# Optimization experiments

Measured on AMD Instinct MI355X. Metric: run time of the kernel, lower is better.

The kernel has to match this reference:

```python
import jax, jax.numpy as jnp
import numpy as np

DIM = 768
HEADS = 12
HEAD_DIM = DIM // HEADS
MAX_LEN = 2048
EPS = 1e-5

def layer_norm(x, w, b):
    mu = jnp.mean(x, axis=-1, keepdims=True)
    var = jnp.var(x, axis=-1, keepdims=True)
    return (x - mu) * jax.lax.rsqrt(var + EPS) * w + b


def setup_inputs() -> dict:
    key = jax.random.key(0)
    ks = jax.random.split(key, 16)
    B, N = 2, 2048
    s = 1.0 / np.sqrt(DIM)
    inp = {
        "visible_features": jax.random.normal(ks[0], (B, N, DIM), jnp.float32),
        "infrared_features": jax.random.normal(ks[1], (B, N, DIM), jnp.float32),
        "wq": jax.random.normal(ks[2], (DIM, DIM), jnp.float32) * s,
        "bq": jnp.zeros((DIM,), jnp.float32),
        "lnq_w": jnp.ones((DIM,), jnp.float32),
        "lnq_b": jnp.zeros((DIM,), jnp.float32),
        "wk": jax.random.normal(ks[3], (DIM, DIM), jnp.float32) * s,
        "bk": jnp.zeros((DIM,), jnp.float32),
        "lnk_w": jnp.ones((DIM,), jnp.float32),
        "lnk_b": jnp.zeros((DIM,), jnp.float32),
        "wv": jax.random.normal(ks[4], (DIM, DIM), jnp.float32) * s,
        "bv": jnp.zeros((DIM,), jnp.float32),
        "lnv_w": jnp.ones((DIM,), jnp.float32),
        "lnv_b": jnp.zeros((DIM,), jnp.float32),
        "pos_emb": jax.random.normal(ks[5], (MAX_LEN, DIM), jnp.float32),
        "wo": jax.random.normal(ks[6], (DIM, DIM), jnp.float32) * s,
        "bo": jnp.zeros((DIM,), jnp.float32),
        "gate_w": jax.random.normal(ks[7], (DIM, 2 * DIM), jnp.float32) * (1.0 / np.sqrt(2 * DIM)),
        "gate_b": jnp.zeros((DIM,), jnp.float32),
        "ln_w": jnp.ones((DIM,), jnp.float32),
        "ln_b": jnp.zeros((DIM,), jnp.float32),
    }
    return inp


def reference(visible_features, infrared_features, wq, bq, lnq_w, lnq_b,
              wk, bk, lnk_w, lnk_b, wv, bv, lnv_w, lnv_b,
              pos_emb, wo, bo, gate_w, gate_b, ln_w, ln_b):
    B, N, _ = visible_features.shape
    scale = HEAD_DIM ** -0.5

    def proj_heads(x, w, b, gw, gb):
        y = layer_norm(x @ w.T + b, gw, gb)  # [B,N,D]
        return y.reshape(B, N, HEADS, HEAD_DIM).transpose(0, 2, 1, 3)  # [B,H,N,d]

    q = proj_heads(infrared_features, wq, bq, lnq_w, lnq_b)
    k = proj_heads(visible_features, wk, bk, lnk_w, lnk_b)
    v = proj_heads(visible_features, wv, bv, lnv_w, lnv_b)

    pos = pos_emb[:N].reshape(1, N, HEADS, HEAD_DIM).transpose(0, 2, 1, 3)  # [1,H,N,d]

    scores = jnp.einsum('bhnd,bhmd->bhnm', q, k) * scale
    scores = scores + jnp.einsum('bhnd,xhmd->bhnm', q, pos)
    attn = jax.nn.softmax(scores, axis=-1)  # dropout is identity in eval

    out = jnp.einsum('bhnm,bhmd->bhnd', attn, v)
    out = out.transpose(0, 2, 1, 3).reshape(B, N, DIM)
    out = out @ wo.T + bo

    gate = jax.nn.sigmoid(jnp.concatenate([visible_features, out], axis=-1) @ gate_w.T + gate_b)
    fused = visible_features * gate + out * (1.0 - gate)
    return layer_norm(fused, ln_w, ln_b)
```

## Files before the change

kernel.cpp:

```cpp
#include <hip/hip_runtime.h>
#include <hip/hip_bf16.h>

#define DIMC 768
#define NSEQ 2048
#define NB 2
#define NH 12
#define HD 64
#define EPSLN 1e-5f

typedef __attribute__((ext_vector_type(8))) short     bf16x8;
typedef __attribute__((ext_vector_type(8))) unsigned short ushort8;
typedef __attribute__((ext_vector_type(4))) unsigned short ushort4v;
typedef __attribute__((ext_vector_type(4))) float     f32x4;

__device__ __forceinline__ unsigned short f2b(float f) {
    union { float f; unsigned u; } x; x.f = f;
    unsigned r = x.u + 0x7fffu + ((x.u >> 16) & 1u);
    return (unsigned short)(r >> 16);
}

#define MFMA16(a, b, c) __builtin_amdgcn_mfma_f32_16x16x32_bf16((a), (b), (c), 0, 0, 0)

__global__ __launch_bounds__(256)
void cast_all_kernel(const float* __restrict__ wq, const float* __restrict__ wk,
                     const float* __restrict__ wv, const float* __restrict__ wo,
                     const float* __restrict__ gw, const float* __restrict__ vis,
                     const float* __restrict__ inf_,
                     unsigned short* __restrict__ o_wq, unsigned short* __restrict__ o_wk,
                     unsigned short* __restrict__ o_wv, unsigned short* __restrict__ o_wo,
                     unsigned short* __restrict__ o_gw, unsigned short* __restrict__ o_vis,
                     unsigned short* __restrict__ o_inf)
{
    const int g = blockIdx.x * 256 + threadIdx.x;
    const int W = 147456;
    const float* src; unsigned short* dst; int off;
    if      (g < 1*W)            { src = wq;   dst = o_wq;  off = g;          }
    else if (g < 2*W)            { src = wk;   dst = o_wk;  off = g - 1*W;    }
    else if (g < 3*W)            { src = wv;   dst = o_wv;  off = g - 2*W;    }
    else if (g < 4*W)            { src = wo;   dst = o_wo;  off = g - 3*W;    }
    else if (g < 4*W + 294912)   { src = gw;   dst = o_gw;  off = g - 4*W;    }
    else if (g < 4*W + 1081344)  { src = vis;  dst = o_vis; off = g - 4*W - 294912; }
    else                         { src = inf_; dst = o_inf; off = g - 4*W - 1081344; }
    f32x4 v = ((const f32x4*)src)[off];
    ushort4v t;
    t[0] = f2b(v[0]); t[1] = f2b(v[1]); t[2] = f2b(v[2]); t[3] = f2b(v[3]);
    ((ushort4v*)dst)[off] = t;
}

template<int ACC, int WBF>
__global__ __launch_bounds__(256)
void gemm_bf16_kernel(const unsigned short* __restrict__ A,
                      const unsigned short* __restrict__ W,
                      const float* __restrict__ bias,
                      float* __restrict__ C,
                      unsigned short* __restrict__ Cb,
                      int ldw)
{
    __shared__ unsigned short As[64][72];
    __shared__ unsigned short Bs[64][72];
    const int m0 = blockIdx.x * 64, n0 = blockIdx.y * 64;
    const int lane = threadIdx.x & 63, wid = threadIdx.x >> 6;
    const int wm = wid >> 1, wn = wid & 1;
    const int r16 = lane & 15, kg = lane >> 4;

    f32x4 acc[2][2] = {};

    const int sr = threadIdx.x >> 2;
    const int sc = (threadIdx.x & 3) * 16;
    const size_t arow = (size_t)(m0 + sr) * DIMC;
    const size_t brow = (size_t)(n0 + sr) * (size_t)ldw;

    for (int k0 = 0; k0 < DIMC; k0 += 64) {
        ushort8 a0 = *(const ushort8*)&A[arow + k0 + sc];
        ushort8 a1 = *(const ushort8*)&A[arow + k0 + sc + 8];
        ushort8 b0 = *(const ushort8*)&W[brow + k0 + sc];
        ushort8 b1 = *(const ushort8*)&W[brow + k0 + sc + 8];
        if (k0) __syncthreads();
        *(ushort8*)&As[sr][sc]     = a0;
        *(ushort8*)&As[sr][sc + 8] = a1;
        *(ushort8*)&Bs[sr][sc]     = b0;
        *(ushort8*)&Bs[sr][sc + 8] = b1;
        __syncthreads();
        #pragma unroll
        for (int ks = 0; ks < 2; ++ks) {
            bf16x8 af0 = *(const bf16x8*)&As[wm*32 +      r16][ks*32 + kg*8];
            bf16x8 af1 = *(const bf16x8*)&As[wm*32 + 16 + r16][ks*32 + kg*8];
            bf16x8 bg0 = *(const bf16x8*)&Bs[wn*32 +      r16][ks*32 + kg*8];
            bf16x8 bg1 = *(const bf16x8*)&Bs[wn*32 + 16 + r16][ks*32 + kg*8];
            acc[0][0] = MFMA16(af0, bg0, acc[0][0]);
            acc[0][1] = MFMA16(af0, bg1, acc[0][1]);
            acc[1][0] = MFMA16(af1, bg0, acc[1][0]);
            acc[1][1] = MFMA16(af1, bg1, acc[1][1]);
        }
    }

    #pragma unroll
    for (int mi = 0; mi < 2; ++mi)
    #pragma unroll
    for (int nj = 0; nj < 2; ++nj) {
        const int gr = m0 + wm*32 + mi*16 + kg*4;
        const int gc = n0 + wn*32 + nj*16 + r16;
        const float bv = bias ? bias[gc] : 0.f;
        #pragma unroll
        for (int r = 0; r < 4; ++r) {
            const size_t idx = (size_t)(gr + r) * DIMC + gc;
            float v = acc[mi][nj][r] + bv;
            if (ACC) v += C[idx];
            C[idx] = v;
            if (WBF) Cb[idx] = f2b(v);
        }
    }
}

template<int MODE>
__global__ __launch_bounds__(256)
void ln_bf16_kernel(const float* __restrict__ Z,
                    const float* __restrict__ w,
                    const float* __restrict__ b,
                    const float* __restrict__ pos,
                    unsigned short* __restrict__ out)
{
    const int row = blockIdx.x;
    const int n = row & (NSEQ - 1);
    float x[3];
    float s = 0.f, q = 0.f;
    #pragma unroll
    for (int u = 0; u < 3; ++u) {
        const int j = threadIdx.x + u * 256;
        x[u] = Z[(size_t)row * DIMC + j];
        s += x[u];
        q += x[u] * x[u];
    }
    #pragma unroll
    for (int off = 32; off > 0; off >>= 1) {
        s += __shfl_down(s, off);
        q += __shfl_down(q, off);
    }
    __shared__ float ls[8];
    const int wv_ = threadIdx.x >> 6;
    if ((threadIdx.x & 63) == 0) { ls[wv_] = s; ls[4 + wv_] = q; }
    __syncthreads();
    if (threadIdx.x == 0) {
        ls[0] = ls[0] + ls[1] + ls[2] + ls[3];
        ls[4] = ls[4] + ls[5] + ls[6] + ls[7];
    }
    __syncthreads();
    const float mu  = ls[0] * (1.f / DIMC);
    const float var = ls[4] * (1.f / DIMC) - mu * mu;
    const float rs  = rsqrtf(var + EPSLN);
    #pragma unroll
    for (int u = 0; u < 3; ++u) {
        const int j = threadIdx.x + u * 256;
        float y = (x[u] - mu) * rs * w[j] + b[j];
        if (MODE == 1) y = y * 0.125f + pos[(size_t)n * DIMC + j];
        out[(size_t)row * DIMC + j] = f2b(y);
    }
}

__global__ __launch_bounds__(256)
void attn_bf16_kernel(const unsigned short* __restrict__ Q,
                      const unsigned short* __restrict__ K,
                      const unsigned short* __restrict__ V,
                      unsigned short* __restrict__ O)
{
    __shared__ unsigned short Ks[64][72];
    __shared__ unsigned short Vt[64][72];
    __shared__ unsigned short Ps[4][16][72];

    const int bh = blockIdx.x;
    const int b = bh / NH, h = bh % NH;
    const int n0 = blockIdx.y * 64;
    const int lane = threadIdx.x & 63, w = threadIdx.x >> 6;
    const int r16 = lane & 15, kg = lane >> 4;

    const size_t base = (size_t)b * NSEQ * DIMC + (size_t)h * HD;

    const size_t qoff = base + (size_t)(n0 + w * 16 + r16) * DIMC + kg * 8;
    bf16x8 aq0 = *(const bf16x8*)&Q[qoff];
    bf16x8 aq1 = *(const bf16x8*)&Q[qoff + 32];

    f32x4 o[4] = {};
    float mrow[4] = {-1e30f, -1e30f, -1e30f, -1e30f};
    float lrow[4] = {};

    for (int m0 = 0; m0 < NSEQ; m0 += 64) {
        __syncthreads();
        {
            const int kv = threadIdx.x >> 2;
            const int c  = (threadIdx.x & 3) * 16;
            const size_t go = base + (size_t)(m0 + kv) * DIMC + c;
            *(ushort8*)&Ks[kv][c]     = *(const ushort8*)&K[go];
            *(ushort8*)&Ks[kv][c + 8] = *(const ushort8*)&K[go + 8];
        }
        {
            const int kv = threadIdx.x & 63;
            const int dg = (threadIdx.x >> 6) * 16;
            const size_t go = base + (size_t)(m0 + kv) * DIMC + dg;
            #pragma unroll
            for (int i = 0; i < 4; ++i) {
                ushort4v v4 = *(const ushort4v*)&V[go + i * 4];
                Vt[dg + i*4 + 0][kv] = v4[0];
                Vt[dg + i*4 + 1][kv] = v4[1];
                Vt[dg + i*4 + 2][kv] = v4[2];
                Vt[dg + i*4 + 3][kv] = v4[3];
            }
        }
        __syncthreads();

        f32x4 sv[4] = {};
        #pragma unroll
        for (int nj = 0; nj < 4; ++nj) {
            bf16x8 kb0 = *(const bf16x8*)&Ks[nj*16 + r16][kg*8];
            bf16x8 kb1 = *(const bf16x8*)&Ks[nj*16 + r16][32 + kg*8];
            sv[nj] = MFMA16(aq0, kb0, sv[nj]);
            sv[nj] = MFMA16(aq1, kb1, sv[nj]);
        }

        #pragma unroll
        for (int r = 0; r < 4; ++r) {
            float mx = fmaxf(fmaxf(sv[0][r], sv[1][r]), fmaxf(sv[2][r], sv[3][r]));
            #pragma unroll
            for (int off = 1; off < 16; off <<= 1)
                mx = fmaxf(mx, __shfl_xor(mx, off));
            const float mnew = fmaxf(mrow[r], mx);
            const float corr = __expf(mrow[r] - mnew);
            float ps = 0.f;
            #pragma unroll
            for (int nj = 0; nj < 4; ++nj) {
                const float p = __expf(sv[nj][r] - mnew);
                sv[nj][r] = p;
                ps += p;
            }
            #pragma unroll
            for (int off = 1; off < 16; off <<= 1)
                ps += __shfl_xor(ps, off);
            lrow[r] = lrow[r] * corr + ps;
            mrow[r] = mnew;
            o[0][r] *= corr; o[1][r] *= corr; o[2][r] *= corr; o[3][r] *= corr;
            const int qr = kg * 4 + r;
            #pragma unroll
            for (int nj = 0; nj < 4; ++nj)
                Ps[w][qr][nj*16 + r16] = f2b(sv[nj][r]);
        }

        bf16x8 pa0 = *(const bf16x8*)&Ps[w][r16][kg*8];
        bf16x8 pa1 = *(const bf16x8*)&Ps[w][r16][32 + kg*8];
        #pragma unroll
        for (int nj = 0; nj < 4; ++nj) {
            bf16x8 vb0 = *(const bf16x8*)&Vt[nj*16 + r16][kg*8];
            bf16x8 vb1 = *(const bf16x8*)&Vt[nj*16 + r16][32 + kg*8];
            o[nj] = MFMA16(pa0, vb0, o[nj]);
            o[nj] = MFMA16(pa1, vb1, o[nj]);
        }
    }

    float inv[4];
    #pragma unroll
    for (int r = 0; r < 4; ++r) inv[r] = 1.f / lrow[r];
    #pragma unroll
    for (int nj = 0; nj < 4; ++nj)
    #pragma unroll
    for (int r = 0; r < 4; ++r) {
        const size_t go = base + (size_t)(n0 + w*16 + kg*4 + r) * DIMC + nj*16 + r16;
        O[go] = f2b(o[nj][r] * inv[r]);
    }
}

__global__ __launch_bounds__(256)
void fuse_ln_kernel(const float* __restrict__ vis,
                    const float* __restrict__ Oc,
                    const float* __restrict__ G,
                    const float* __restrict__ w,
                    const float* __restrict__ b,
                    float* __restrict__ out)
{
    const int row = blockIdx.x;
    float f[3];
    float s = 0.f, q = 0.f;
    #pragma unroll
    for (int u = 0; u < 3; ++u) {
        const size_t idx = (size_t)row * DIMC + threadIdx.x + u * 256;
        const float vv = vis[idx];
        const float oo = Oc[idx];
        const float gg = 1.f / (1.f + __expf(-G[idx]));
        f[u] = vv * gg + oo * (1.f - gg);
        s += f[u];
        q += f[u] * f[u];
    }
    #pragma unroll
    for (int off = 32; off > 0; off >>= 1) {
        s += __shfl_down(s, off);
        q += __shfl_down(q, off);
    }
    __shared__ float ls[8];
    const int wv_ = threadIdx.x >> 6;
    if ((threadIdx.x & 63) == 0) { ls[wv_] = s; ls[4 + wv_] = q; }
    __syncthreads();
    if (threadIdx.x == 0) {
        ls[0] = ls[0] + ls[1] + ls[2] + ls[3];
        ls[4] = ls[4] + ls[5] + ls[6] + ls[7];
    }
    __syncthreads();
    const float mu  = ls[0] * (1.f / DIMC);
    const float var = ls[4] * (1.f / DIMC) - mu * mu;
    const float rs  = rsqrtf(var + EPSLN);
    #pragma unroll
    for (int u = 0; u < 3; ++u) {
        const int j = threadIdx.x + u * 256;
        out[(size_t)row * DIMC + j] = (f[u] - mu) * rs * w[j] + b[j];
    }
}

extern "C" void kernel_launch(void* const* d_in, const int* in_sizes, int n_in,
                              void* d_out, int out_size, void* d_ws, size_t ws_size,
                              hipStream_t stream)
{
    const float* vis  = (const float*)d_in[0];
    const float* inf_ = (const float*)d_in[1];
    const float* wq   = (const float*)d_in[2];
    const float* bq   = (const float*)d_in[3];
    const float* lnqw = (const float*)d_in[4];
    const float* lnqb = (const float*)d_in[5];
    const float* wk   = (const float*)d_in[6];
    const float* bk   = (const float*)d_in[7];
    const float* lnkw = (const float*)d_in[8];
    const float* lnkb = (const float*)d_in[9];
    const float* wv   = (const float*)d_in[10];
    const float* bv   = (const float*)d_in[11];
    const float* lnvw = (const float*)d_in[12];
    const float* lnvb = (const float*)d_in[13];
    const float* pos  = (const float*)d_in[14];
    const float* wo   = (const float*)d_in[15];
    const float* bo   = (const float*)d_in[16];
    const float* gw   = (const float*)d_in[17];
    const float* gb   = (const float*)d_in[18];
    const float* lnw  = (const float*)d_in[19];
    const float* lnb  = (const float*)d_in[20];

    const size_t WEL = 589824;
    const size_t GEL = 1179648;
    const size_t BUF = (size_t)NB * NSEQ * DIMC;

    unsigned short* p = (unsigned short*)d_ws;
    unsigned short* wq_b  = p;  p += WEL;
    unsigned short* wk_b  = p;  p += WEL;
    unsigned short* wv_b  = p;  p += WEL;
    unsigned short* wo_b  = p;  p += WEL;
    unsigned short* gw_b  = p;  p += GEL;
    unsigned short* vis_b = p;  p += BUF;
    unsigned short* inf_b = p;  p += BUF;
    unsigned short* q_b   = p;  p += BUF;
    unsigned short* k_b   = p;  p += BUF;
    unsigned short* v_b   = p;  p += BUF;
    unsigned short* oc_b  = p;  p += BUF;
    float* Oc  = (float*)k_b;
    float* tmp = (float*)d_out;
    float* G   = (float*)d_out;

    dim3 blk(256);
    dim3 ggemm(64, 12);

    cast_all_kernel<<<dim3(9600), blk, 0, stream>>>(
        wq, wk, wv, wo, gw, vis, inf_,
        wq_b, wk_b, wv_b, wo_b, gw_b, vis_b, inf_b);

    gemm_bf16_kernel<0,0><<<ggemm, blk, 0, stream>>>(inf_b, wq_b, bq, tmp, nullptr, DIMC);
    ln_bf16_kernel<0><<<dim3(4096), blk, 0, stream>>>(tmp, lnqw, lnqb, nullptr, q_b);
    gemm_bf16_kernel<0,0><<<ggemm, blk, 0, stream>>>(vis_b, wk_b, bk, tmp, nullptr, DIMC);
    ln_bf16_kernel<1><<<dim3(4096), blk, 0, stream>>>(tmp, lnkw, lnkb, pos, k_b);
    gemm_bf16_kernel<0,0><<<ggemm, blk, 0, stream>>>(vis_b, wv_b, bv, tmp, nullptr, DIMC);
    ln_bf16_kernel<0><<<dim3(4096), blk, 0, stream>>>(tmp, lnvw, lnvb, nullptr, v_b);

    attn_bf16_kernel<<<dim3(NB * NH, NSEQ / 64), blk, 0, stream>>>(q_b, k_b, v_b, q_b);

    gemm_bf16_kernel<0,1><<<ggemm, blk, 0, stream>>>(q_b, wo_b, bo, Oc, oc_b, DIMC);

    gemm_bf16_kernel<0,0><<<ggemm, blk, 0, stream>>>(vis_b, gw_b, gb, G, nullptr, 2 * DIMC);
    gemm_bf16_kernel<1,0><<<ggemm, blk, 0, stream>>>(oc_b, gw_b + DIMC, nullptr, G, nullptr, 2 * DIMC);

    fuse_ln_kernel<<<dim3(4096), blk, 0, stream>>>(vis, Oc, G, lnw, lnb, (float*)d_out);
}
```

Before: 335.7 us.

## Merge K/V/gate projections into one GEMM, enlarge tiles, streamline attention softmax

Concatenates the wk, wv and visible-half gate weights into one matrix so a single 128x128-tile GEMM produces K and V pre-activations (stored as bf16) plus the gate partial. It adds direct global-to-LDS loads and MFMA priority hints in the GEMM, and accumulates the oc-half gate product in place. In attention, the swapped MFMA operand order lets each lane own one key column, so row max and sum need only two cross-lane shuffles. It also uses exp2 with log2e folded into K, and packs P to bf16 with a hardware convert. This cuts launches and per-row shuffle work, but stores K/V pre-LN values in bf16 and relies on the unswizzled 64-wide LDS layout, which may cause bank conflicts.

```diff
diff --git a/kernel.cpp b/kernel.cpp
--- a/kernel.cpp
+++ b/kernel.cpp
@@ -7,114 +7,169 @@
 #define NH 12
 #define HD 64
 #define EPSLN 1e-5f
-
-typedef __attribute__((ext_vector_type(8))) short     bf16x8;
+#define LOG2E 1.44269504f
+
+typedef __attribute__((ext_vector_type(8))) short          bf16x8;
 typedef __attribute__((ext_vector_type(8))) unsigned short ushort8;
 typedef __attribute__((ext_vector_type(4))) unsigned short ushort4v;
-typedef __attribute__((ext_vector_type(4))) float     f32x4;
+typedef __attribute__((ext_vector_type(4))) float          f32x4;
+typedef unsigned int u32;
 
 __device__ __forceinline__ unsigned short f2b(float f) {
     union { float f; unsigned u; } x; x.f = f;
     unsigned r = x.u + 0x7fffu + ((x.u >> 16) & 1u);
     return (unsigned short)(r >> 16);
 }
+__device__ __forceinline__ float b2f(unsigned short v) {
+    union { unsigned u; float f; } x; x.u = ((u32)v) << 16; return x.f;
+}
 
 #define MFMA16(a, b, c) __builtin_amdgcn_mfma_f32_16x16x32_bf16((a), (b), (c), 0, 0, 0)
+
+__device__ __forceinline__ void gl_lds16(const unsigned short* g, unsigned short* l) {
+    __builtin_amdgcn_global_load_lds(
+        (const __attribute__((address_space(1))) u32*)(const void*)g,
+        (__attribute__((address_space(3))) u32*)(void*)l, 16, 0, 0);
+}
+
+#define G_WQ   147456
+#define G_MW   442368
+#define G_G2   147456
+#define G_WO   147456
+#define G_VIS  786432
+#define G_INF  786432
+#define G_BF_TOTAL (G_WQ + G_MW + G_G2 + G_WO + G_VIS + G_INF)
+#define G_BIAS 576
+#define G_ALL  (G_BF_TOTAL + G_BIAS)
 
 __global__ __launch_bounds__(256)
 void cast_all_kernel(const float* __restrict__ wq, const float* __restrict__ wk,
-                     const float* __restrict__ wv, const float* __restrict__ wo,
-                     const float* __restrict__ gw, const float* __restrict__ vis,
-                     const float* __restrict__ inf_,
-                     unsigned short* __restrict__ o_wq, unsigned short* __restrict__ o_wk,
-                     unsigned short* __restrict__ o_wv, unsigned short* __restrict__ o_wo,
-                     unsigned short* __restrict__ o_gw, unsigned short* __restrict__ o_vis,
-                     unsigned short* __restrict__ o_inf)
+                     const float* __restrict__ wv, const float* __restrict__ gw,
+                     const float* __restrict__ wo,
+                     const float* __restrict__ bk, const float* __restrict__ bv,
+                     const float* __restrict__ gb,
+                     const float* __restrict__ vis, const float* __restrict__ inf_,
+                     unsigned short* __restrict__ o_wq, unsigned short* __restrict__ o_mw,
+                     unsigned short* __restrict__ o_g2, unsigned short* __restrict__ o_wo,
+                     unsigned short* __restrict__ o_vis, unsigned short* __restrict__ o_inf,
+                     float* __restrict__ o_biasc)
 {
     const int g = blockIdx.x * 256 + threadIdx.x;
-    const int W = 147456;
-    const float* src; unsigned short* dst; int off;
-    if      (g < 1*W)            { src = wq;   dst = o_wq;  off = g;          }
-    else if (g < 2*W)            { src = wk;   dst = o_wk;  off = g - 1*W;    }
-    else if (g < 3*W)            { src = wv;   dst = o_wv;  off = g - 2*W;    }
-    else if (g < 4*W)            { src = wo;   dst = o_wo;  off = g - 3*W;    }
-    else if (g < 4*W + 294912)   { src = gw;   dst = o_gw;  off = g - 4*W;    }
-    else if (g < 4*W + 1081344)  { src = vis;  dst = o_vis; off = g - 4*W - 294912; }
-    else                         { src = inf_; dst = o_inf; off = g - 4*W - 1081344; }
-    f32x4 v = ((const f32x4*)src)[off];
+    if (g >= G_ALL) return;
+    if (g >= G_BF_TOTAL) {
+        const int e0 = (g - G_BF_TOTAL) * 4;
+        float4 r;
+        float* pr = (float*)&r;
+        #pragma unroll
+        for (int t = 0; t < 4; ++t) {
+            const int e = e0 + t;
+            pr[t] = (e < 768) ? bk[e] : (e < 1536) ? bv[e - 768] : gb[e - 1536];
+        }
+        *(float4*)&o_biasc[e0] = r;
+        return;
+    }
+    const float* src; unsigned short* dst; int soff, doff = 0;
+    int gg = g;
+    if (gg < G_WQ) { src = wq; dst = o_wq; soff = gg; doff = gg; }
+    else if ((gg -= G_WQ) < G_MW) {
+        const int row = gg / 192, c4 = gg % 192;
+        dst = o_mw; doff = gg;
+        if      (row < 768)  { src = wk; soff = row * 192 + c4; }
+        else if (row < 1536) { src = wv; soff = (row - 768) * 192 + c4; }
+        else                 { src = gw; soff = (row - 1536) * 384 + c4; }
+    }
+    else if ((gg -= G_MW) < G_G2) {
+        const int row = gg / 192, c4 = gg % 192;
+        src = gw; soff = row * 384 + 192 + c4; dst = o_g2; doff = gg;
+    }
+    else if ((gg -= G_G2) < G_WO)  { src = wo;   dst = o_wo;  soff = gg; doff = gg; }
+    else if ((gg -= G_WO) < G_VIS) { src = vis;  dst = o_vis; soff = gg; doff = gg; }
+    else { gg -= G_VIS;              src = inf_; dst = o_inf; soff = gg; doff = gg; }
+    f32x4 v = ((const f32x4*)src)[soff];
     ushort4v t;
     t[0] = f2b(v[0]); t[1] = f2b(v[1]); t[2] = f2b(v[2]); t[3] = f2b(v[3]);
-    ((ushort4v*)dst)[off] = t;
-}
-
-template<int ACC, int WBF>
+    ((ushort4v*)dst)[doff] = t;
+}
+
+template<int MODE>
 __global__ __launch_bounds__(256)
-void gemm_bf16_kernel(const unsigned short* __restrict__ A,
-                      const unsigned short* __restrict__ W,
-                      const float* __restrict__ bias,
-                      float* __restrict__ C,
-                      unsigned short* __restrict__ Cb,
-                      int ldw)
-{
-    __shared__ unsigned short As[64][72];
-    __shared__ unsigned short Bs[64][72];
-    const int m0 = blockIdx.x * 64, n0 = blockIdx.y * 64;
+void gemm128(const unsigned short* __restrict__ A,
+             const unsigned short* __restrict__ W,
+             const float* __restrict__ bias,
+             float* __restrict__ Cf,
+             unsigned short* __restrict__ Cb)
+{
+    __shared__ unsigned short As[128 * 64];
+    __shared__ unsigned short Bs[128 * 64];
+    const int m0 = blockIdx.x * 128, n0 = blockIdx.y * 128;
     const int lane = threadIdx.x & 63, wid = threadIdx.x >> 6;
     const int wm = wid >> 1, wn = wid & 1;
     const int r16 = lane & 15, kg = lane >> 4;
-
-    f32x4 acc[2][2] = {};
-
-    const int sr = threadIdx.x >> 2;
-    const int sc = (threadIdx.x & 3) * 16;
-    const size_t arow = (size_t)(m0 + sr) * DIMC;
-    const size_t brow = (size_t)(n0 + sr) * (size_t)ldw;
+    const int lrow = lane >> 3;
+    const int lcol = (lane & 7) * 8;
+
+    f32x4 acc[4][4] = {};
 
     for (int k0 = 0; k0 < DIMC; k0 += 64) {
-        ushort8 a0 = *(const ushort8*)&A[arow + k0 + sc];
-        ushort8 a1 = *(const ushort8*)&A[arow + k0 + sc + 8];
-        ushort8 b0 = *(const ushort8*)&W[brow + k0 + sc];
-        ushort8 b1 = *(const ushort8*)&W[brow + k0 + sc + 8];
         if (k0) __syncthreads();
-        *(ushort8*)&As[sr][sc]     = a0;
-        *(ushort8*)&As[sr][sc + 8] = a1;
-        *(ushort8*)&Bs[sr][sc]     = b0;
-        *(ushort8*)&Bs[sr][sc + 8] = b1;
+        #pragma unroll
+        for (int i = 0; i < 4; ++i) {
+            const int c = wid * 4 + i;
+            const int row = c * 8 + lrow;
+            gl_lds16(&A[(size_t)(m0 + row) * DIMC + k0 + lcol], &As[c * 512]);
+            gl_lds16(&W[(size_t)(n0 + row) * DIMC + k0 + lcol], &Bs[c * 512]);
+        }
         __syncthreads();
         #pragma unroll
         for (int ks = 0; ks < 2; ++ks) {
-            bf16x8 af0 = *(const bf16x8*)&As[wm*32 +      r16][ks*32 + kg*8];
-            bf16x8 af1 = *(const bf16x8*)&As[wm*32 + 16 + r16][ks*32 + kg*8];
-            bf16x8 bg0 = *(const bf16x8*)&Bs[wn*32 +      r16][ks*32 + kg*8];
-            bf16x8 bg1 = *(const bf16x8*)&Bs[wn*32 + 16 + r16][ks*32 + kg*8];
-            acc[0][0] = MFMA16(af0, bg0, acc[0][0]);
-            acc[0][1] = MFMA16(af0, bg1, acc[0][1]);
-            acc[1][0] = MFMA16(af1, bg0, acc[1][0]);
-            acc[1][1] = MFMA16(af1, bg1, acc[1][1]);
-        }
-    }
-
-    #pragma unroll
-    for (int mi = 0; mi < 2; ++mi)
-    #pragma unroll
-    for (int nj = 0; nj < 2; ++nj) {
-        const int gr = m0 + wm*32 + mi*16 + kg*4;
-        const int gc = n0 + wn*32 + nj*16 + r16;
-        const float bv = bias ? bias[gc] : 0.f;
+            bf16x8 af[4], bg[4];
+            #pragma unroll
+            for (int mi = 0; mi < 4; ++mi)
+                af[mi] = *(const bf16x8*)&As[(wm * 64 + mi * 16 + r16) * 64 + ks * 32 + kg * 8];
+            #pragma unroll
+            for (int nj = 0; nj < 4; ++nj)
+                bg[nj] = *(const bf16x8*)&Bs[(wn * 64 + nj * 16 + r16) * 64 + ks * 32 + kg * 8];
+            __builtin_amdgcn_s_setprio(1);
+            #pragma unroll
+            for (int mi = 0; mi < 4; ++mi)
+                #pragma unroll
+                for (int nj = 0; nj < 4; ++nj)
+                    acc[mi][nj] = MFMA16(af[mi], bg[nj], acc[mi][nj]);
+            __builtin_amdgcn_s_setprio(0);
+        }
+    }
+
+    #pragma unroll
+    for (int mi = 0; mi < 4; ++mi)
+    #pragma unroll
+    for (int nj = 0; nj < 4; ++nj) {
+        const int gr = m0 + wm * 64 + mi * 16 + kg * 4;
+        const int gc = n0 + wn * 64 + nj * 16 + r16;
+        const float bvl = (MODE == 3) ? 0.f : bias[gc];
         #pragma unroll
         for (int r = 0; r < 4; ++r) {
-            const size_t idx = (size_t)(gr + r) * DIMC + gc;
-            float v = acc[mi][nj][r] + bv;
-            if (ACC) v += C[idx];
-            C[idx] = v;
-            if (WBF) Cb[idx] = f2b(v);
-        }
-    }
-}
-
-template<int MODE>
+            const float val = acc[mi][nj][r] + bvl;
+            if (MODE == 0) {
+                Cf[(size_t)(gr + r) * DIMC + gc] = val;
+            } else if (MODE == 1) {
+                if (gc < 1536) Cb[(size_t)(gr + r) * 1536 + gc] = f2b(val);
+                else           Cf[(size_t)(gr + r) * DIMC + (gc - 1536)] = val;
+            } else if (MODE == 2) {
+                const size_t idx = (size_t)(gr + r) * DIMC + gc;
+                Cf[idx] = val;
+                Cb[idx] = f2b(val);
+            } else {
+                const size_t idx = (size_t)(gr + r) * DIMC + gc;
+                Cf[idx] += val;
+            }
+        }
+    }
+}
+
+template<int INBF, int MODE>
 __global__ __launch_bounds__(256)
-void ln_bf16_kernel(const float* __restrict__ Z,
+void ln_bf16_kernel(const void* __restrict__ Zv,
+                    int ld,
                     const float* __restrict__ w,
                     const float* __restrict__ b,
                     const float* __restrict__ pos,
@@ -127,7 +182,8 @@
     #pragma unroll
     for (int u = 0; u < 3; ++u) {
         const int j = threadIdx.x + u * 256;
-        x[u] = Z[(size_t)row * DIMC + j];
+        if (INBF) x[u] = b2f(((const unsigned short*)Zv)[(size_t)row * ld + j]);
+        else      x[u] = ((const float*)Zv)[(size_t)row * ld + j];
         s += x[u];
         q += x[u] * x[u];
     }
@@ -152,7 +208,7 @@
     for (int u = 0; u < 3; ++u) {
         const int j = threadIdx.x + u * 256;
         float y = (x[u] - mu) * rs * w[j] + b[j];
-        if (MODE == 1) y = y * 0.125f + pos[(size_t)n * DIMC + j];
+        if (MODE == 1) y = y * (0.125f * LOG2E) + pos[(size_t)n * DIMC + j] * LOG2E;
         out[(size_t)row * DIMC + j] = f2b(y);
     }
 }
@@ -180,8 +236,7 @@
     bf16x8 aq1 = *(const bf16x8*)&Q[qoff + 32];
 
     f32x4 o[4] = {};
-    float mrow[4] = {-1e30f, -1e30f, -1e30f, -1e30f};
-    float lrow[4] = {};
+    float m_run = -1e30f, l_run = 0.f;
 
     for (int m0 = 0; m0 < NSEQ; m0 += 64) {
         __syncthreads();
@@ -199,70 +254,89 @@
             #pragma unroll
             for (int i = 0; i < 4; ++i) {
                 ushort4v v4 = *(const ushort4v*)&V[go + i * 4];
-                Vt[dg + i*4 + 0][kv] = v4[0];
-                Vt[dg + i*4 + 1][kv] = v4[1];
-                Vt[dg + i*4 + 2][kv] = v4[2];
-                Vt[dg + i*4 + 3][kv] = v4[3];
+                Vt[dg + i * 4 + 0][kv] = v4[0];
+                Vt[dg + i * 4 + 1][kv] = v4[1];
+                Vt[dg + i * 4 + 2][kv] = v4[2];
+                Vt[dg + i * 4 + 3][kv] = v4[3];
             }
         }
         __syncthreads();
 
-        f32x4 sv[4] = {};
+        f32x4 sv[4];
+        #pragma unroll
+        for (int f = 0; f < 4; ++f) sv[f] = (f32x4){0.f, 0.f, 0.f, 0.f};
+        __builtin_amdgcn_s_setprio(1);
+        #pragma unroll
+        for (int f = 0; f < 4; ++f) {
+            bf16x8 kb0 = *(const bf16x8*)&Ks[f * 16 + r16][kg * 8];
+            bf16x8 kb1 = *(const bf16x8*)&Ks[f * 16 + r16][32 + kg * 8];
+            sv[f] = MFMA16(kb0, aq0, sv[f]);
+            sv[f] = MFMA16(kb1, aq1, sv[f]);
+        }
+        __builtin_amdgcn_s_setprio(0);
+
+        float mt = sv[0][0];
+        #pragma unroll
+        for (int f = 0; f < 4; ++f)
+            #pragma unroll
+            for (int j = 0; j < 4; ++j)
+                mt = fmaxf(mt, sv[f][j]);
+        mt = fmaxf(mt, __shfl_xor(mt, 16));
+        mt = fmaxf(mt, __shfl_xor(mt, 32));
+        const float mnew = fmaxf(m_run, mt);
+        const float corr = exp2f(m_run - mnew);
+        float p[4][4];
+        float st = 0.f;
+        #pragma unroll
+        for (int f = 0; f < 4; ++f)
+            #pragma unroll
+            for (int j = 0; j < 4; ++j) {
+                p[f][j] = exp2f(sv[f][j] - mnew);
+                st += p[f][j];
+            }
+        st += __shfl_xor(st, 16);
+        st += __shfl_xor(st, 32);
+        l_run = l_run * corr + st;
+        m_run = mnew;
+
+        #pragma unroll
+        for (int f = 0; f < 4; ++f) {
+            u32 w0, w1;
+            asm("v_cvt_pk_bf16_f32 %0, %1, %2" : "=v"(w0) : "v"(p[f][0]), "v"(p[f][1]));
+            asm("v_cvt_pk_bf16_f32 %0, %1, %2" : "=v"(w1) : "v"(p[f][2]), "v"(p[f][3]));
+            *(u32*)&Ps[w][r16][kg * 4 + 16 * f]     = w0;
+            *(u32*)&Ps[w][r16][kg * 4 + 2 + 16 * f] = w1;
+        }
+
+        #pragma unroll
+        for (int jj = 0; jj < 4; ++jj) {
+            const float cq = __shfl(corr, kg * 4 + jj);
+            o[0][jj] *= cq; o[1][jj] *= cq; o[2][jj] *= cq; o[3][jj] *= cq;
+        }
+
+        bf16x8 pa0 = *(const bf16x8*)&Ps[w][r16][kg * 8];
+        bf16x8 pa1 = *(const bf16x8*)&Ps[w][r16][32 + kg * 8];
+        __builtin_amdgcn_s_setprio(1);
         #pragma unroll
         for (int nj = 0; nj < 4; ++nj) {
-            bf16x8 kb0 = *(const bf16x8*)&Ks[nj*16 + r16][kg*8];
-            bf16x8 kb1 = *(const bf16x8*)&Ks[nj*16 + r16][32 + kg*8];
-            sv[nj] = MFMA16(aq0, kb0, sv[nj]);
-            sv[nj] = MFMA16(aq1, kb1, sv[nj]);
-        }
-
-        #pragma unroll
-        for (int r = 0; r < 4; ++r) {
-            float mx = fmaxf(fmaxf(sv[0][r], sv[1][r]), fmaxf(sv[2][r], sv[3][r]));
-            #pragma unroll
-            for (int off = 1; off < 16; off <<= 1)
-                mx = fmaxf(mx, __shfl_xor(mx, off));
-            const float mnew = fmaxf(mrow[r], mx);
-            const float corr = __expf(mrow[r] - mnew);
-            float ps = 0.f;
-            #pragma unroll
-            for (int nj = 0; nj < 4; ++nj) {
-                const float p = __expf(sv[nj][r] - mnew);
-                sv[nj][r] = p;
-                ps += p;
-            }
-            #pragma unroll
-            for (int off = 1; off < 16; off <<= 1)
-                ps += __shfl_xor(ps, off);
-            lrow[r] = lrow[r] * corr + ps;
-            mrow[r] = mnew;
-            o[0][r] *= corr; o[1][r] *= corr; o[2][r] *= corr; o[3][r] *= corr;
-            const int qr = kg * 4 + r;
-            #pragma unroll
-            for (int nj = 0; nj < 4; ++nj)
-                Ps[w][qr][nj*16 + r16] = f2b(sv[nj][r]);
-        }
-
-        bf16x8 pa0 = *(const bf16x8*)&Ps[w][r16][kg*8];
-        bf16x8 pa1 = *(const bf16x8*)&Ps[w][r16][32 + kg*8];
-        #pragma unroll
-        for (int nj = 0; nj < 4; ++nj) {
-            bf16x8 vb0 = *(const bf16x8*)&Vt[nj*16 + r16][kg*8];
-            bf16x8 vb1 = *(const bf16x8*)&Vt[nj*16 + r16][32 + kg*8];
+            bf16x8 vb0 = *(const bf16x8*)&Vt[nj * 16 + r16][kg * 8];
+            bf16x8 vb1 = *(const bf16x8*)&Vt[nj * 16 + r16][32 + kg * 8];
             o[nj] = MFMA16(pa0, vb0, o[nj]);
             o[nj] = MFMA16(pa1, vb1, o[nj]);
         }
-    }
-
-    float inv[4];
-    #pragma unroll
-    for (int r = 0; r < 4; ++r) inv[r] = 1.f / lrow[r];
+        __builtin_amdgcn_s_setprio(0);
+    }
+
+    float linv[4];
+    #pragma unroll
+    for (int jj = 0; jj < 4; ++jj)
+        linv[jj] = 1.f / __shfl(l_run, kg * 4 + jj);
     #pragma unroll
     for (int nj = 0; nj < 4; ++nj)
     #pragma unroll
-    for (int r = 0; r < 4; ++r) {
-        const size_t go = base + (size_t)(n0 + w*16 + kg*4 + r) * DIMC + nj*16 + r16;
-        O[go] = f2b(o[nj][r] * inv[r]);
+    for (int jj = 0; jj < 4; ++jj) {
+        const size_t go = base + (size_t)(n0 + w * 16 + kg * 4 + jj) * DIMC + nj * 16 + r16;
+        O[go] = f2b(o[nj][jj] * linv[jj]);
     }
 }
 
@@ -338,45 +412,44 @@
     const float* lnb  = (const float*)d_in[20];
 
     const size_t WEL = 589824;
-    const size_t GEL = 1179648;
+    const size_t MWEL = 1769472;
     const size_t BUF = (size_t)NB * NSEQ * DIMC;
 
     unsigned short* p = (unsigned short*)d_ws;
     unsigned short* wq_b  = p;  p += WEL;
-    unsigned short* wk_b  = p;  p += WEL;
-    unsigned short* wv_b  = p;  p += WEL;
+    unsigned short* mw_b  = p;  p += MWEL;
+    unsigned short* g2_b  = p;  p += WEL;
     unsigned short* wo_b  = p;  p += WEL;
-    unsigned short* gw_b  = p;  p += GEL;
     unsigned short* vis_b = p;  p += BUF;
     unsigned short* inf_b = p;  p += BUF;
     unsigned short* q_b   = p;  p += BUF;
     unsigned short* k_b   = p;  p += BUF;
     unsigned short* v_b   = p;  p += BUF;
-    unsigned short* oc_b  = p;  p += BUF;
+    unsigned short* kvpre = p;  p += 2 * BUF;
+    float* biasc = (float*)p;
+
+    float* Gd  = (float*)d_out;
     float* Oc  = (float*)k_b;
-    float* tmp = (float*)d_out;
-    float* G   = (float*)d_out;
+    unsigned short* oc_b = inf_b;
 
     dim3 blk(256);
-    dim3 ggemm(64, 12);
-
-    cast_all_kernel<<<dim3(9600), blk, 0, stream>>>(
-        wq, wk, wv, wo, gw, vis, inf_,
-        wq_b, wk_b, wv_b, wo_b, gw_b, vis_b, inf_b);
-
-    gemm_bf16_kernel<0,0><<<ggemm, blk, 0, stream>>>(inf_b, wq_b, bq, tmp, nullptr, DIMC);
-    ln_bf16_kernel<0><<<dim3(4096), blk, 0, stream>>>(tmp, lnqw, lnqb, nullptr, q_b);
-    gemm_bf16_kernel<0,0><<<ggemm, blk, 0, stream>>>(vis_b, wk_b, bk, tmp, nullptr, DIMC);
-    ln_bf16_kernel<1><<<dim3(4096), blk, 0, stream>>>(tmp, lnkw, lnkb, pos, k_b);
-    gemm_bf16_kernel<0,0><<<ggemm, blk, 0, stream>>>(vis_b, wv_b, bv, tmp, nullptr, DIMC);
-    ln_bf16_kernel<0><<<dim3(4096), blk, 0, stream>>>(tmp, lnvw, lnvb, nullptr, v_b);
+
+    cast_all_kernel<<<dim3((G_ALL + 255) / 256), blk, 0, stream>>>(
+        wq, wk, wv, gw, wo, bk, bv, gb, vis, inf_,
+        wq_b, mw_b, g2_b, wo_b, vis_b, inf_b, biasc);
+
+    gemm128<0><<<dim3(32, 6), blk, 0, stream>>>(inf_b, wq_b, bq, Gd, nullptr);
+    ln_bf16_kernel<0, 0><<<dim3(4096), blk, 0, stream>>>(Gd, DIMC, lnqw, lnqb, nullptr, q_b);
+
+    gemm128<1><<<dim3(32, 18), blk, 0, stream>>>(vis_b, mw_b, biasc, Gd, kvpre);
+    ln_bf16_kernel<1, 1><<<dim3(4096), blk, 0, stream>>>(kvpre, 1536, lnkw, lnkb, pos, k_b);
+    ln_bf16_kernel<1, 0><<<dim3(4096), blk, 0, stream>>>(kvpre + DIMC, 1536, lnvw, lnvb, nullptr, v_b);
 
     attn_bf16_kernel<<<dim3(NB * NH, NSEQ / 64), blk, 0, stream>>>(q_b, k_b, v_b, q_b);
 
-    gemm_bf16_kernel<0,1><<<ggemm, blk, 0, stream>>>(q_b, wo_b, bo, Oc, oc_b, DIMC);
-
-    gemm_bf16_kernel<0,0><<<ggemm, blk, 0, stream>>>(vis_b, gw_b, gb, G, nullptr, 2 * DIMC);
-    gemm_bf16_kernel<1,0><<<ggemm, blk, 0, stream>>>(oc_b, gw_b + DIMC, nullptr, G, nullptr, 2 * DIMC);
-
-    fuse_ln_kernel<<<dim3(4096), blk, 0, stream>>>(vis, Oc, G, lnw, lnb, (float*)d_out);
-}
+    gemm128<2><<<dim3(32, 6), blk, 0, stream>>>(q_b, wo_b, bo, Oc, oc_b);
+
+    gemm128<3><<<dim3(32, 6), blk, 0, stream>>>(oc_b, g2_b, nullptr, Gd, nullptr);
+
+    fuse_ln_kernel<<<dim3(4096), blk, 0, stream>>>(vis, Oc, Gd, lnw, lnb, (float*)d_out);
+}
```

After: 326.1 us. 1.03x faster.
